# Performance work log

Measured on AMD Instinct MI355X. Metric: run time of the kernel, lower is better.

The kernel has to match this reference:

```python
import jax, jax.numpy as jnp
import numpy as np

N, C, H, W = 16, 256, 128, 128
TC = max(8, C // 32)  # temp_c
EPS = 1e-5


def setup_inputs() -> dict:
    key = jax.random.key(0)
    ks = jax.random.split(key, 10)
    x = jax.random.normal(ks[0], (N, C, H, W), jnp.float32)
    # conv1: 1x1, C -> TC (weight squeezed to [TC, C])
    w1 = jax.random.normal(ks[1], (TC, C), jnp.float32) * 0.05
    b1 = jnp.zeros((TC,), jnp.float32)
    # BatchNorm2d (inference form)
    bn_gamma = jnp.ones((TC,), jnp.float32)
    bn_beta = jnp.zeros((TC,), jnp.float32)
    bn_mean = jnp.zeros((TC,), jnp.float32)
    bn_var = jnp.ones((TC,), jnp.float32)
    # conv2: kernel (1,2), TC -> C, squeezed to [C, TC, 2]
    w2 = jax.random.normal(ks[2], (C, TC, 2), jnp.float32) * 0.1
    b2 = jnp.zeros((C,), jnp.float32)
    # conv3: kernel (2,1), TC -> C, squeezed to [C, TC, 2]
    w3 = jax.random.normal(ks[3], (C, TC, 2), jnp.float32) * 0.1
    b3 = jnp.zeros((C,), jnp.float32)
    # conv4: kernel (1,2), TC -> C, squeezed to [C, TC, 2]
    w4 = jax.random.normal(ks[4], (C, TC, 2), jnp.float32) * 0.1
    b4 = jnp.zeros((C,), jnp.float32)
    return dict(x=x, w1=w1, b1=b1, bn_gamma=bn_gamma, bn_beta=bn_beta,
                bn_mean=bn_mean, bn_var=bn_var, w2=w2, b2=b2, w3=w3, b3=b3,
                w4=w4, b4=b4)


def reference(x, w1, b1, bn_gamma, bn_beta, bn_mean, bn_var,
              w2, b2, w3, b3, w4, b4):
    n, c, Hh, Ww = x.shape
    # avg/max pools along W (per-row), H (per-col), and global (per-channel)
    cat_h = jnp.stack([x.mean(3), x.max(3)], axis=-1)            # [n,c,H,2]
    cat_w = jnp.stack([x.mean(2), x.max(2)], axis=-1)            # [n,c,W,2]
    cat_c = jnp.stack([x.mean((2, 3)), x.max((2, 3))], -1)[:, :, None, :]  # [n,c,1,2]
    x_cat = jnp.concatenate([cat_h, cat_w, cat_c], axis=2)       # [n,c,H+W+1,2]
    # 1x1 conv + BN (inference) + h_swish
    y = jnp.einsum('ncsk,tc->ntsk', x_cat, w1) + b1[None, :, None, None]
    inv = bn_gamma / jnp.sqrt(bn_var + EPS)
    y = (y - bn_mean[None, :, None, None]) * inv[None, :, None, None] \
        + bn_beta[None, :, None, None]
    y = y * jnp.clip(y + 3.0, 0.0, 6.0) / 6.0                    # h_swish
    # split
    xh = y[:, :, :Hh, :]               # [n,tc,H,2]
    xw = y[:, :, Hh:Hh + Ww, :]        # [n,tc,W,2]
    xc = y[:, :, Hh + Ww, :]           # [n,tc,2]
    # tiny convs (kernels collapse to contractions over (tc, k)) + sigmoid
    a_h = jax.nn.sigmoid(jnp.einsum('nthk,otk->noh', xh, w2) + b2[None, :, None])  # [n,C,H]
    a_w = jax.nn.sigmoid(jnp.einsum('ntwk,otk->now', xw, w3) + b3[None, :, None])  # [n,C,W]
    a_c = jax.nn.sigmoid(jnp.einsum('ntk,otk->no', xc, w4) + b4[None, :])          # [n,C]
    return x * a_w[:, :, None, :] * a_h[:, :, :, None] * a_c[:, :, None, None]
```

## Files before the change

### kernel.cpp

```cpp
#include <hip/hip_runtime.h>
#include <math.h>

#define N_ 16
#define C_ 256
#define H_ 128
#define W_ 128
#define TC_ 8
#define S_ 257
#define EPS_ 1e-5f
#define NBLK 512
#define BPN 32
#define PPB 8

#define XCT_OFF  0
#define AH_OFF   2105344
#define AW_OFF   (AH_OFF + 524288)
#define Y256_OFF (AW_OFF + 524288)
#define CNT_OFF  (Y256_OFF + 256)

typedef float f4n __attribute__((ext_vector_type(4)));

__device__ __forceinline__ void nbar(unsigned* c, unsigned target) {
    __syncthreads();
    if (threadIdx.x == 0) {
        __hip_atomic_fetch_add(c, 1u, __ATOMIC_RELEASE, __HIP_MEMORY_SCOPE_AGENT);
        while (__hip_atomic_load(c, __ATOMIC_RELAXED, __HIP_MEMORY_SCOPE_AGENT) < target)
            __builtin_amdgcn_s_sleep(16);
        (void)__hip_atomic_load(c, __ATOMIC_ACQUIRE, __HIP_MEMORY_SCOPE_AGENT);
    }
    __syncthreads();
}

__global__ __launch_bounds__(256, 2) void mega(
    const float* __restrict__ x,
    const float* __restrict__ w1, const float* __restrict__ b1,
    const float* __restrict__ gam, const float* __restrict__ bet,
    const float* __restrict__ mu, const float* __restrict__ var,
    const float* __restrict__ w2, const float* __restrict__ b2,
    const float* __restrict__ w3, const float* __restrict__ b3,
    const float* __restrict__ w4, const float* __restrict__ b4,
    float* __restrict__ xcat, float* __restrict__ ahg, float* __restrict__ awg,
    float* __restrict__ y256g, unsigned* __restrict__ cnt,
    float* __restrict__ out)
{
    const int b = blockIdx.x;
    const int n = b >> 5, cg = b & 31, c0 = cg * 8;
    const int tid = threadIdx.x;
    __shared__ __align__(16) float smf[9472];

    {
        float2 (*rowp)[33] = reinterpret_cast<float2(*)[33]>(smf);
        float4* scr_s = reinterpret_cast<float4*>(smf + 8448);
        float4* scr_m = reinterpret_cast<float4*>(smf + 8960);
        const int rg = tid >> 5;

        for (int u = 0; u < PPB; ++u) {
            const int p = b * PPB + u;
            const float4* xt = reinterpret_cast<const float4*>(x) + (size_t)p * 4096;
            float2* xcat2 = reinterpret_cast<float2*>(xcat) + (size_t)p * S_;

            float4 cs = make_float4(0.f, 0.f, 0.f, 0.f);
            float4 cm = make_float4(-INFINITY, -INFINITY, -INFINITY, -INFINITY);

            #pragma unroll
            for (int k = 0; k < 16; ++k) {
                const float4 v = xt[k * 256 + tid];
                cs.x += v.x; cs.y += v.y; cs.z += v.z; cs.w += v.w;
                cm.x = fmaxf(cm.x, v.x); cm.y = fmaxf(cm.y, v.y);
                cm.z = fmaxf(cm.z, v.z); cm.w = fmaxf(cm.w, v.w);
                const float rs = (v.x + v.y) + (v.z + v.w);
                const float rm = fmaxf(fmaxf(v.x, v.y), fmaxf(v.z, v.w));
                rowp[k * 8 + rg][tid & 31] = make_float2(rs, rm);
            }

            cs.x += __shfl_xor(cs.x, 32); cs.y += __shfl_xor(cs.y, 32);
            cs.z += __shfl_xor(cs.z, 32); cs.w += __shfl_xor(cs.w, 32);
            cm.x = fmaxf(cm.x, __shfl_xor(cm.x, 32));
            cm.y = fmaxf(cm.y, __shfl_xor(cm.y, 32));
            cm.z = fmaxf(cm.z, __shfl_xor(cm.z, 32));
            cm.w = fmaxf(cm.w, __shfl_xor(cm.w, 32));

            const int wv = tid >> 6, ln = tid & 63;
            if (ln < 32) { scr_s[wv * 32 + ln] = cs; scr_m[wv * 32 + ln] = cm; }
            __syncthreads();

            if (tid >= 128) {
                const int h = tid - 128;
                float2 q0 = rowp[h][0];
                float s = q0.x, m = q0.y;
                #pragma unroll
                for (int j = 1; j < 32; ++j) {
                    const float2 q = rowp[h][j];
                    s += q.x; m = fmaxf(m, q.y);
                }
                xcat2[h] = make_float2(s * (1.f / 128.f), m);
            }

            if (tid < 32) {
                const float4 s0 = scr_s[tid],      s1 = scr_s[32 + tid],
                             s2 = scr_s[64 + tid], s3 = scr_s[96 + tid];
                const float4 m0 = scr_m[tid],      m1 = scr_m[32 + tid],
                             m2 = scr_m[64 + tid], m3 = scr_m[96 + tid];
                float4 S, M;
                S.x = (s0.x + s1.x) + (s2.x + s3.x);
                S.y = (s0.y + s1.y) + (s2.y + s3.y);
                S.z = (s0.z + s1.z) + (s2.z + s3.z);
                S.w = (s0.w + s1.w) + (s2.w + s3.w);
                M.x = fmaxf(fmaxf(m0.x, m1.x), fmaxf(m2.x, m3.x));
                M.y = fmaxf(fmaxf(m0.y, m1.y), fmaxf(m2.y, m3.y));
                M.z = fmaxf(fmaxf(m0.z, m1.z), fmaxf(m2.z, m3.z));
                M.w = fmaxf(fmaxf(m0.w, m1.w), fmaxf(m2.w, m3.w));

                const int w0 = 4 * tid;
                xcat2[128 + w0 + 0] = make_float2(S.x * (1.f / 128.f), M.x);
                xcat2[128 + w0 + 1] = make_float2(S.y * (1.f / 128.f), M.y);
                xcat2[128 + w0 + 2] = make_float2(S.z * (1.f / 128.f), M.z);
                xcat2[128 + w0 + 3] = make_float2(S.w * (1.f / 128.f), M.w);

                float gs = (S.x + S.y) + (S.z + S.w);
                float gm = fmaxf(fmaxf(M.x, M.y), fmaxf(M.z, M.w));
                #pragma unroll
                for (int m = 16; m >= 1; m >>= 1) {
                    gs += __shfl_xor(gs, m);
                    gm = fmaxf(gm, __shfl_xor(gm, m));
                }
                if (tid == 0) xcat2[256] = make_float2(gs * (1.f / 16384.f), gm);
            }
            __syncthreads();
        }
    }

    nbar(cnt + n * 64, BPN);

    {
        float* w1s = smf;
        float* red = smf + 2048;
        float* ys  = smf + 6272;
        const float2* xc2 = reinterpret_cast<const float2*>(xcat) + (size_t)n * C_ * S_;
        const int s0 = cg * 8;

        for (int i = tid; i < TC_ * C_; i += 256) w1s[i] = w1[i];
        __syncthreads();

        {
            const int cgrp = tid >> 3, si = tid & 7;
            const int s = s0 + si;
            float acc[16];
            #pragma unroll
            for (int j = 0; j < 16; ++j) acc[j] = 0.f;
            #pragma unroll
            for (int i = 0; i < 8; ++i) {
                const int c = cgrp * 8 + i;
                const float2 v = xc2[c * S_ + s];
                #pragma unroll
                for (int t = 0; t < TC_; ++t) {
                    const float w = w1s[t * C_ + c];
                    acc[t * 2 + 0] += v.x * w;
                    acc[t * 2 + 1] += v.y * w;
                }
            }
            #pragma unroll
            for (int j = 0; j < 16; ++j) red[(si * 16 + j) * 33 + cgrp] = acc[j];
        }
        __syncthreads();

        if (tid < 128) {
            const int si2 = tid >> 4, j = tid & 15, t = j >> 1;
            float z = 0.f;
            #pragma unroll
            for (int g = 0; g < 32; ++g) z += red[(si2 * 16 + j) * 33 + g];
            const float inv = gam[t] * rsqrtf(var[t] + EPS_);
            float y = (z + b1[t] - mu[t]) * inv + bet[t];
            y = y * fminf(fmaxf(y + 3.f, 0.f), 6.f) * (1.f / 6.f);
            ys[si2 * 17 + j] = y;
        }
        __syncthreads();

        if (cg == BPN - 1) {
            const int c = tid;
            const float2 v = xc2[c * S_ + 256];
            float pj[16];
            #pragma unroll
            for (int t = 0; t < TC_; ++t) {
                const float w = w1s[t * C_ + c];
                pj[t * 2 + 0] = v.x * w;
                pj[t * 2 + 1] = v.y * w;
            }
            __syncthreads();
            float* red2 = smf;
            float* redB = smf + 4400;
            #pragma unroll
            for (int j = 0; j < 16; ++j) red2[tid * 17 + j] = pj[j];
            __syncthreads();
            {
                const int g = tid >> 4, j = tid & 15;
                float z = 0.f;
                #pragma unroll
                for (int m = 0; m < 16; ++m) z += red2[(g * 16 + m) * 17 + j];
                redB[j * 17 + g] = z;
            }
            __syncthreads();
            if (tid < 16) {
                const int j = tid, t = j >> 1;
                float z = 0.f;
                #pragma unroll
                for (int g = 0; g < 16; ++g) z += redB[j * 17 + g];
                const float inv = gam[t] * rsqrtf(var[t] + EPS_);
                float y = (z + b1[t] - mu[t]) * inv + bet[t];
                y = y * fminf(fmaxf(y + 3.f, 0.f), 6.f) * (1.f / 6.f);
                y256g[n * 16 + j] = y;
            }
            __syncthreads();
        }

        {
            const int o = tid;
            const bool is_h = (cg < 16);
            const float* wX = is_h ? w2 : w3;
            const float zb = is_h ? b2[o] : b3[o];
            float4 wr[4];
            const float4* wv = reinterpret_cast<const float4*>(wX + o * 16);
            #pragma unroll
            for (int q = 0; q < 4; ++q) wr[q] = wv[q];

            float r[8];
            #pragma unroll
            for (int si = 0; si < 8; ++si) {
                float z = zb;
                #pragma unroll
                for (int q = 0; q < 4; ++q) {
                    z += ys[si * 17 + q * 4 + 0] * wr[q].x
                       + ys[si * 17 + q * 4 + 1] * wr[q].y
                       + ys[si * 17 + q * 4 + 2] * wr[q].z
                       + ys[si * 17 + q * 4 + 3] * wr[q].w;
                }
                r[si] = 1.f / (1.f + expf(-z));
            }
            float* og = is_h ? (ahg + (size_t)(n * C_ + o) * H_ + s0)
                             : (awg + (size_t)(n * C_ + o) * W_ + (s0 - 128));
            *reinterpret_cast<float4*>(og)     = make_float4(r[0], r[1], r[2], r[3]);
            *reinterpret_cast<float4*>(og + 4) = make_float4(r[4], r[5], r[6], r[7]);
        }
    }

    nbar(cnt + n * 64 + 32, BPN);

    float* acs = smf;
    float* ahl = smf + 16;
    float* awl = smf + 1040;
    {
        if (tid < 8) {
            const int o = c0 + tid;
            float z = b4[o];
            #pragma unroll
            for (int j = 0; j < 16; ++j) z += y256g[n * 16 + j] * w4[o * 16 + j];
            acs[tid] = 1.f / (1.f + expf(-z));
        }
        __syncthreads();

        for (int idx = tid; idx < 8 * 128; idx += 256) {
            const int u = idx >> 7, h = idx & 127, o = c0 + u;
            ahl[idx] = acs[u] * ahg[(size_t)(n * C_ + o) * H_ + h];
            awl[idx] = awg[(size_t)(n * C_ + o) * W_ + h];
        }
        __syncthreads();
    }
    {
        const float4* awv = reinterpret_cast<const float4*>(awl);
        for (int u = 0; u < PPB; ++u) {
            const int p = b * PPB + u;
            const f4n* x4 = reinterpret_cast<const f4n*>(x) + (size_t)p * 4096;
            f4n* o4 = reinterpret_cast<f4n*>(out) + (size_t)p * 4096;

            const float4 a = awv[u * 32 + (tid & 31)];
            #pragma unroll
            for (int k = 0; k < 16; ++k) {
                const int i4 = k * 256 + tid;
                f4n v = x4[i4];
                const float s = ahl[u * 128 + k * 8 + (tid >> 5)];
                v.x *= s * a.x; v.y *= s * a.y; v.z *= s * a.z; v.w *= s * a.w;
                __builtin_nontemporal_store(v, &o4[i4]);
            }
        }
    }
}

extern "C" void kernel_launch(void* const* d_in, const int* in_sizes, int n_in,
                              void* d_out, int out_size, void* d_ws, size_t ws_size,
                              hipStream_t stream) {
    const float* x   = (const float*)d_in[0];
    const float* w1  = (const float*)d_in[1];
    const float* b1  = (const float*)d_in[2];
    const float* gam = (const float*)d_in[3];
    const float* bet = (const float*)d_in[4];
    const float* mu  = (const float*)d_in[5];
    const float* var = (const float*)d_in[6];
    const float* w2  = (const float*)d_in[7];
    const float* b2  = (const float*)d_in[8];
    const float* w3  = (const float*)d_in[9];
    const float* b3  = (const float*)d_in[10];
    const float* w4  = (const float*)d_in[11];
    const float* b4  = (const float*)d_in[12];

    float* ws    = (float*)d_ws;
    float* xcat  = ws + XCT_OFF;
    float* ahg   = ws + AH_OFF;
    float* awg   = ws + AW_OFF;
    float* y256g = ws + Y256_OFF;
    unsigned* cnt = (unsigned*)(ws + CNT_OFF);
    float* out   = (float*)d_out;

    hipMemsetAsync((void*)cnt, 0, 16 * 64 * sizeof(unsigned), stream);
    mega<<<NBLK, 256, 0, stream>>>(x, w1, b1, gam, bet, mu, var,
                                   w2, b2, w3, b3, w4, b4,
                                   xcat, ahg, awg, y256g, cnt, out);
}
```

Measured before the change: 175.5 us.

## Split persistent mega-kernel into three kernels replacing atomic grid barriers

Replaces the single persistent kernel, which used per-batch atomic spin barriers between phases, with three separate launches: pooling statistics, attention-vector computation, and the final apply. This removes the memset and the spin-wait barrier overhead, and lets kernels 2 and 3 use smaller shared memory for higher occupancy. In exchange it adds two extra launch boundaries and loses the chance that x stays in cache between the stats and apply phases in the same block.

```diff
diff --git a/kernel.cpp b/kernel.cpp
--- a/kernel.cpp
+++ b/kernel.cpp
@@ -16,271 +16,266 @@
 #define AH_OFF   2105344
 #define AW_OFF   (AH_OFF + 524288)
 #define Y256_OFF (AW_OFF + 524288)
-#define CNT_OFF  (Y256_OFF + 256)
 
 typedef float f4n __attribute__((ext_vector_type(4)));
 
-__device__ __forceinline__ void nbar(unsigned* c, unsigned target) {
-    __syncthreads();
-    if (threadIdx.x == 0) {
-        __hip_atomic_fetch_add(c, 1u, __ATOMIC_RELEASE, __HIP_MEMORY_SCOPE_AGENT);
-        while (__hip_atomic_load(c, __ATOMIC_RELAXED, __HIP_MEMORY_SCOPE_AGENT) < target)
-            __builtin_amdgcn_s_sleep(16);
-        (void)__hip_atomic_load(c, __ATOMIC_ACQUIRE, __HIP_MEMORY_SCOPE_AGENT);
-    }
-    __syncthreads();
+__global__ __launch_bounds__(256, 2) void k1_stats(
+    const float* __restrict__ x, float* __restrict__ xcat)
+{
+    const int b = blockIdx.x;
+    const int tid = threadIdx.x;
+    __shared__ __align__(16) float smf[9472];
+
+    float2 (*rowp)[33] = reinterpret_cast<float2(*)[33]>(smf);
+    float4* scr_s = reinterpret_cast<float4*>(smf + 8448);
+    float4* scr_m = reinterpret_cast<float4*>(smf + 8960);
+    const int rg = tid >> 5;
+
+    for (int u = 0; u < PPB; ++u) {
+        const int p = b * PPB + u;
+        const float4* xt = reinterpret_cast<const float4*>(x) + (size_t)p * 4096;
+        float2* xcat2 = reinterpret_cast<float2*>(xcat) + (size_t)p * S_;
+
+        float4 cs = make_float4(0.f, 0.f, 0.f, 0.f);
+        float4 cm = make_float4(-INFINITY, -INFINITY, -INFINITY, -INFINITY);
+
+        #pragma unroll
+        for (int k = 0; k < 16; ++k) {
+            const float4 v = xt[k * 256 + tid];
+            cs.x += v.x; cs.y += v.y; cs.z += v.z; cs.w += v.w;
+            cm.x = fmaxf(cm.x, v.x); cm.y = fmaxf(cm.y, v.y);
+            cm.z = fmaxf(cm.z, v.z); cm.w = fmaxf(cm.w, v.w);
+            const float rs = (v.x + v.y) + (v.z + v.w);
+            const float rm = fmaxf(fmaxf(v.x, v.y), fmaxf(v.z, v.w));
+            rowp[k * 8 + rg][tid & 31] = make_float2(rs, rm);
+        }
+
+        cs.x += __shfl_xor(cs.x, 32); cs.y += __shfl_xor(cs.y, 32);
+        cs.z += __shfl_xor(cs.z, 32); cs.w += __shfl_xor(cs.w, 32);
+        cm.x = fmaxf(cm.x, __shfl_xor(cm.x, 32));
+        cm.y = fmaxf(cm.y, __shfl_xor(cm.y, 32));
+        cm.z = fmaxf(cm.z, __shfl_xor(cm.z, 32));
+        cm.w = fmaxf(cm.w, __shfl_xor(cm.w, 32));
+
+        const int wv = tid >> 6, ln = tid & 63;
+        if (ln < 32) { scr_s[wv * 32 + ln] = cs; scr_m[wv * 32 + ln] = cm; }
+        __syncthreads();
+
+        if (tid >= 128) {
+            const int h = tid - 128;
+            float2 q0 = rowp[h][0];
+            float s = q0.x, m = q0.y;
+            #pragma unroll
+            for (int j = 1; j < 32; ++j) {
+                const float2 q = rowp[h][j];
+                s += q.x; m = fmaxf(m, q.y);
+            }
+            xcat2[h] = make_float2(s * (1.f / 128.f), m);
+        }
+
+        if (tid < 32) {
+            const float4 s0 = scr_s[tid],      s1 = scr_s[32 + tid],
+                         s2 = scr_s[64 + tid], s3 = scr_s[96 + tid];
+            const float4 m0 = scr_m[tid],      m1 = scr_m[32 + tid],
+                         m2 = scr_m[64 + tid], m3 = scr_m[96 + tid];
+            float4 S, M;
+            S.x = (s0.x + s1.x) + (s2.x + s3.x);
+            S.y = (s0.y + s1.y) + (s2.y + s3.y);
+            S.z = (s0.z + s1.z) + (s2.z + s3.z);
+            S.w = (s0.w + s1.w) + (s2.w + s3.w);
+            M.x = fmaxf(fmaxf(m0.x, m1.x), fmaxf(m2.x, m3.x));
+            M.y = fmaxf(fmaxf(m0.y, m1.y), fmaxf(m2.y, m3.y));
+            M.z = fmaxf(fmaxf(m0.z, m1.z), fmaxf(m2.z, m3.z));
+            M.w = fmaxf(fmaxf(m0.w, m1.w), fmaxf(m2.w, m3.w));
+
+            const int w0 = 4 * tid;
+            xcat2[128 + w0 + 0] = make_float2(S.x * (1.f / 128.f), M.x);
+            xcat2[128 + w0 + 1] = make_float2(S.y * (1.f / 128.f), M.y);
+            xcat2[128 + w0 + 2] = make_float2(S.z * (1.f / 128.f), M.z);
+            xcat2[128 + w0 + 3] = make_float2(S.w * (1.f / 128.f), M.w);
+
+            float gs = (S.x + S.y) + (S.z + S.w);
+            float gm = fmaxf(fmaxf(M.x, M.y), fmaxf(M.z, M.w));
+            #pragma unroll
+            for (int m = 16; m >= 1; m >>= 1) {
+                gs += __shfl_xor(gs, m);
+                gm = fmaxf(gm, __shfl_xor(gm, m));
+            }
+            if (tid == 0) xcat2[256] = make_float2(gs * (1.f / 16384.f), gm);
+        }
+        __syncthreads();
+    }
 }
 
-__global__ __launch_bounds__(256, 2) void mega(
-    const float* __restrict__ x,
+__global__ __launch_bounds__(256, 2) void k2_attn(
+    const float* __restrict__ xcat,
     const float* __restrict__ w1, const float* __restrict__ b1,
     const float* __restrict__ gam, const float* __restrict__ bet,
     const float* __restrict__ mu, const float* __restrict__ var,
     const float* __restrict__ w2, const float* __restrict__ b2,
     const float* __restrict__ w3, const float* __restrict__ b3,
+    float* __restrict__ ahg, float* __restrict__ awg, float* __restrict__ y256g)
+{
+    const int b = blockIdx.x;
+    const int n = b >> 5, cg = b & 31;
+    const int tid = threadIdx.x;
+    __shared__ __align__(16) float smf[6448];
+
+    float* w1s = smf;
+    float* red = smf + 2048;
+    float* ys  = smf + 6272;
+    const float2* xc2 = reinterpret_cast<const float2*>(xcat) + (size_t)n * C_ * S_;
+    const int s0 = cg * 8;
+
+    for (int i = tid; i < TC_ * C_; i += 256) w1s[i] = w1[i];
+    __syncthreads();
+
+    {
+        const int cgrp = tid >> 3, si = tid & 7;
+        const int s = s0 + si;
+        float acc[16];
+        #pragma unroll
+        for (int j = 0; j < 16; ++j) acc[j] = 0.f;
+        #pragma unroll
+        for (int i = 0; i < 8; ++i) {
+            const int c = cgrp * 8 + i;
+            const float2 v = xc2[c * S_ + s];
+            #pragma unroll
+            for (int t = 0; t < TC_; ++t) {
+                const float w = w1s[t * C_ + c];
+                acc[t * 2 + 0] += v.x * w;
+                acc[t * 2 + 1] += v.y * w;
+            }
+        }
+        #pragma unroll
+        for (int j = 0; j < 16; ++j) red[(si * 16 + j) * 33 + cgrp] = acc[j];
+    }
+    __syncthreads();
+
+    if (tid < 128) {
+        const int si2 = tid >> 4, j = tid & 15, t = j >> 1;
+        float z = 0.f;
+        #pragma unroll
+        for (int g = 0; g < 32; ++g) z += red[(si2 * 16 + j) * 33 + g];
+        const float inv = gam[t] * rsqrtf(var[t] + EPS_);
+        float y = (z + b1[t] - mu[t]) * inv + bet[t];
+        y = y * fminf(fmaxf(y + 3.f, 0.f), 6.f) * (1.f / 6.f);
+        ys[si2 * 17 + j] = y;
+    }
+    __syncthreads();
+
+    if (cg == BPN - 1) {
+        const int c = tid;
+        const float2 v = xc2[c * S_ + 256];
+        float pj[16];
+        #pragma unroll
+        for (int t = 0; t < TC_; ++t) {
+            const float w = w1s[t * C_ + c];
+            pj[t * 2 + 0] = v.x * w;
+            pj[t * 2 + 1] = v.y * w;
+        }
+        __syncthreads();
+        float* red2 = smf;
+        float* redB = smf + 4400;
+        #pragma unroll
+        for (int j = 0; j < 16; ++j) red2[tid * 17 + j] = pj[j];
+        __syncthreads();
+        {
+            const int g = tid >> 4, j = tid & 15;
+            float z = 0.f;
+            #pragma unroll
+            for (int m = 0; m < 16; ++m) z += red2[(g * 16 + m) * 17 + j];
+            redB[j * 17 + g] = z;
+        }
+        __syncthreads();
+        if (tid < 16) {
+            const int j = tid, t = j >> 1;
+            float z = 0.f;
+            #pragma unroll
+            for (int g = 0; g < 16; ++g) z += redB[j * 17 + g];
+            const float inv = gam[t] * rsqrtf(var[t] + EPS_);
+            float y = (z + b1[t] - mu[t]) * inv + bet[t];
+            y = y * fminf(fmaxf(y + 3.f, 0.f), 6.f) * (1.f / 6.f);
+            y256g[n * 16 + j] = y;
+        }
+        __syncthreads();
+    }
+
+    {
+        const int o = tid;
+        const bool is_h = (cg < 16);
+        const float* wX = is_h ? w2 : w3;
+        const float zb = is_h ? b2[o] : b3[o];
+        float4 wr[4];
+        const float4* wv = reinterpret_cast<const float4*>(wX + o * 16);
+        #pragma unroll
+        for (int q = 0; q < 4; ++q) wr[q] = wv[q];
+
+        float r[8];
+        #pragma unroll
+        for (int si = 0; si < 8; ++si) {
+            float z = zb;
+            #pragma unroll
+            for (int q = 0; q < 4; ++q) {
+                z += ys[si * 17 + q * 4 + 0] * wr[q].x
+                   + ys[si * 17 + q * 4 + 1] * wr[q].y
+                   + ys[si * 17 + q * 4 + 2] * wr[q].z
+                   + ys[si * 17 + q * 4 + 3] * wr[q].w;
+            }
+            r[si] = 1.f / (1.f + expf(-z));
+        }
+        float* og = is_h ? (ahg + (size_t)(n * C_ + o) * H_ + s0)
+                         : (awg + (size_t)(n * C_ + o) * W_ + (s0 - 128));
+        *reinterpret_cast<float4*>(og)     = make_float4(r[0], r[1], r[2], r[3]);
+        *reinterpret_cast<float4*>(og + 4) = make_float4(r[4], r[5], r[6], r[7]);
+    }
+}
+
+__global__ __launch_bounds__(256, 2) void k3_apply(
+    const float* __restrict__ x,
     const float* __restrict__ w4, const float* __restrict__ b4,
-    float* __restrict__ xcat, float* __restrict__ ahg, float* __restrict__ awg,
-    float* __restrict__ y256g, unsigned* __restrict__ cnt,
-    float* __restrict__ out)
+    const float* __restrict__ ahg, const float* __restrict__ awg,
+    const float* __restrict__ y256g, float* __restrict__ out)
 {
     const int b = blockIdx.x;
     const int n = b >> 5, cg = b & 31, c0 = cg * 8;
     const int tid = threadIdx.x;
-    __shared__ __align__(16) float smf[9472];
-
-    {
-        float2 (*rowp)[33] = reinterpret_cast<float2(*)[33]>(smf);
-        float4* scr_s = reinterpret_cast<float4*>(smf + 8448);
-        float4* scr_m = reinterpret_cast<float4*>(smf + 8960);
-        const int rg = tid >> 5;
-
-        for (int u = 0; u < PPB; ++u) {
-            const int p = b * PPB + u;
-            const float4* xt = reinterpret_cast<const float4*>(x) + (size_t)p * 4096;
-            float2* xcat2 = reinterpret_cast<float2*>(xcat) + (size_t)p * S_;
-
-            float4 cs = make_float4(0.f, 0.f, 0.f, 0.f);
-            float4 cm = make_float4(-INFINITY, -INFINITY, -INFINITY, -INFINITY);
-
-            #pragma unroll
-            for (int k = 0; k < 16; ++k) {
-                const float4 v = xt[k * 256 + tid];
-                cs.x += v.x; cs.y += v.y; cs.z += v.z; cs.w += v.w;
-                cm.x = fmaxf(cm.x, v.x); cm.y = fmaxf(cm.y, v.y);
-                cm.z = fmaxf(cm.z, v.z); cm.w = fmaxf(cm.w, v.w);
-                const float rs = (v.x + v.y) + (v.z + v.w);
-                const float rm = fmaxf(fmaxf(v.x, v.y), fmaxf(v.z, v.w));
-                rowp[k * 8 + rg][tid & 31] = make_float2(rs, rm);
-            }
-
-            cs.x += __shfl_xor(cs.x, 32); cs.y += __shfl_xor(cs.y, 32);
-            cs.z += __shfl_xor(cs.z, 32); cs.w += __shfl_xor(cs.w, 32);
-            cm.x = fmaxf(cm.x, __shfl_xor(cm.x, 32));
-            cm.y = fmaxf(cm.y, __shfl_xor(cm.y, 32));
-            cm.z = fmaxf(cm.z, __shfl_xor(cm.z, 32));
-            cm.w = fmaxf(cm.w, __shfl_xor(cm.w, 32));
-
-            const int wv = tid >> 6, ln = tid & 63;
-            if (ln < 32) { scr_s[wv * 32 + ln] = cs; scr_m[wv * 32 + ln] = cm; }
-            __syncthreads();
-
-            if (tid >= 128) {
-                const int h = tid - 128;
-                float2 q0 = rowp[h][0];
-                float s = q0.x, m = q0.y;
-                #pragma unroll
-                for (int j = 1; j < 32; ++j) {
-                    const float2 q = rowp[h][j];
-                    s += q.x; m = fmaxf(m, q.y);
-                }
-                xcat2[h] = make_float2(s * (1.f / 128.f), m);
-            }
-
-            if (tid < 32) {
-                const float4 s0 = scr_s[tid],      s1 = scr_s[32 + tid],
-                             s2 = scr_s[64 + tid], s3 = scr_s[96 + tid];
-                const float4 m0 = scr_m[tid],      m1 = scr_m[32 + tid],
-                             m2 = scr_m[64 + tid], m3 = scr_m[96 + tid];
-                float4 S, M;
-                S.x = (s0.x + s1.x) + (s2.x + s3.x);
-                S.y = (s0.y + s1.y) + (s2.y + s3.y);
-                S.z = (s0.z + s1.z) + (s2.z + s3.z);
-                S.w = (s0.w + s1.w) + (s2.w + s3.w);
-                M.x = fmaxf(fmaxf(m0.x, m1.x), fmaxf(m2.x, m3.x));
-                M.y = fmaxf(fmaxf(m0.y, m1.y), fmaxf(m2.y, m3.y));
-                M.z = fmaxf(fmaxf(m0.z, m1.z), fmaxf(m2.z, m3.z));
-                M.w = fmaxf(fmaxf(m0.w, m1.w), fmaxf(m2.w, m3.w));
-
-                const int w0 = 4 * tid;
-                xcat2[128 + w0 + 0] = make_float2(S.x * (1.f / 128.f), M.x);
-                xcat2[128 + w0 + 1] = make_float2(S.y * (1.f / 128.f), M.y);
-                xcat2[128 + w0 + 2] = make_float2(S.z * (1.f / 128.f), M.z);
-                xcat2[128 + w0 + 3] = make_float2(S.w * (1.f / 128.f), M.w);
-
-                float gs = (S.x + S.y) + (S.z + S.w);
-                float gm = fmaxf(fmaxf(M.x, M.y), fmaxf(M.z, M.w));
-                #pragma unroll
-                for (int m = 16; m >= 1; m >>= 1) {
-                    gs += __shfl_xor(gs, m);
-                    gm = fmaxf(gm, __shfl_xor(gm, m));
-                }
-                if (tid == 0) xcat2[256] = make_float2(gs * (1.f / 16384.f), gm);
-            }
-            __syncthreads();
-        }
-    }
-
-    nbar(cnt + n * 64, BPN);
-
-    {
-        float* w1s = smf;
-        float* red = smf + 2048;
-        float* ys  = smf + 6272;
-        const float2* xc2 = reinterpret_cast<const float2*>(xcat) + (size_t)n * C_ * S_;
-        const int s0 = cg * 8;
-
-        for (int i = tid; i < TC_ * C_; i += 256) w1s[i] = w1[i];
-        __syncthreads();
-
-        {
-            const int cgrp = tid >> 3, si = tid & 7;
-            const int s = s0 + si;
-            float acc[16];
-            #pragma unroll
-            for (int j = 0; j < 16; ++j) acc[j] = 0.f;
-            #pragma unroll
-            for (int i = 0; i < 8; ++i) {
-                const int c = cgrp * 8 + i;
-                const float2 v = xc2[c * S_ + s];
-                #pragma unroll
-                for (int t = 0; t < TC_; ++t) {
-                    const float w = w1s[t * C_ + c];
-                    acc[t * 2 + 0] += v.x * w;
-                    acc[t * 2 + 1] += v.y * w;
-                }
-            }
-            #pragma unroll
-            for (int j = 0; j < 16; ++j) red[(si * 16 + j) * 33 + cgrp] = acc[j];
-        }
-        __syncthreads();
-
-        if (tid < 128) {
-            const int si2 = tid >> 4, j = tid & 15, t = j >> 1;
-            float z = 0.f;
-            #pragma unroll
-            for (int g = 0; g < 32; ++g) z += red[(si2 * 16 + j) * 33 + g];
-            const float inv = gam[t] * rsqrtf(var[t] + EPS_);
-            float y = (z + b1[t] - mu[t]) * inv + bet[t];
-            y = y * fminf(fmaxf(y + 3.f, 0.f), 6.f) * (1.f / 6.f);
-            ys[si2 * 17 + j] = y;
-        }
-        __syncthreads();
-
-        if (cg == BPN - 1) {
-            const int c = tid;
-            const float2 v = xc2[c * S_ + 256];
-            float pj[16];
-            #pragma unroll
-            for (int t = 0; t < TC_; ++t) {
-                const float w = w1s[t * C_ + c];
-                pj[t * 2 + 0] = v.x * w;
-                pj[t * 2 + 1] = v.y * w;
-            }
-            __syncthreads();
-            float* red2 = smf;
-            float* redB = smf + 4400;
-            #pragma unroll
-            for (int j = 0; j < 16; ++j) red2[tid * 17 + j] = pj[j];
-            __syncthreads();
-            {
-                const int g = tid >> 4, j = tid & 15;
-                float z = 0.f;
-                #pragma unroll
-                for (int m = 0; m < 16; ++m) z += red2[(g * 16 + m) * 17 + j];
-                redB[j * 17 + g] = z;
-            }
-            __syncthreads();
-            if (tid < 16) {
-                const int j = tid, t = j >> 1;
-                float z = 0.f;
-                #pragma unroll
-                for (int g = 0; g < 16; ++g) z += redB[j * 17 + g];
-                const float inv = gam[t] * rsqrtf(var[t] + EPS_);
-                float y = (z + b1[t] - mu[t]) * inv + bet[t];
-                y = y * fminf(fmaxf(y + 3.f, 0.f), 6.f) * (1.f / 6.f);
-                y256g[n * 16 + j] = y;
-            }
-            __syncthreads();
-        }
-
-        {
-            const int o = tid;
-            const bool is_h = (cg < 16);
-            const float* wX = is_h ? w2 : w3;
-            const float zb = is_h ? b2[o] : b3[o];
-            float4 wr[4];
-            const float4* wv = reinterpret_cast<const float4*>(wX + o * 16);
-            #pragma unroll
-            for (int q = 0; q < 4; ++q) wr[q] = wv[q];
-
-            float r[8];
-            #pragma unroll
-            for (int si = 0; si < 8; ++si) {
-                float z = zb;
-                #pragma unroll
-                for (int q = 0; q < 4; ++q) {
-                    z += ys[si * 17 + q * 4 + 0] * wr[q].x
-                       + ys[si * 17 + q * 4 + 1] * wr[q].y
-                       + ys[si * 17 + q * 4 + 2] * wr[q].z
-                       + ys[si * 17 + q * 4 + 3] * wr[q].w;
-                }
-                r[si] = 1.f / (1.f + expf(-z));
-            }
-            float* og = is_h ? (ahg + (size_t)(n * C_ + o) * H_ + s0)
-                             : (awg + (size_t)(n * C_ + o) * W_ + (s0 - 128));
-            *reinterpret_cast<float4*>(og)     = make_float4(r[0], r[1], r[2], r[3]);
-            *reinterpret_cast<float4*>(og + 4) = make_float4(r[4], r[5], r[6], r[7]);
-        }
-    }
-
-    nbar(cnt + n * 64 + 32, BPN);
+    __shared__ __align__(16) float smf[2064];
 
     float* acs = smf;
     float* ahl = smf + 16;
     float* awl = smf + 1040;
-    {
-        if (tid < 8) {
-            const int o = c0 + tid;
-            float z = b4[o];
-            #pragma unroll
-            for (int j = 0; j < 16; ++j) z += y256g[n * 16 + j] * w4[o * 16 + j];
-            acs[tid] = 1.f / (1.f + expf(-z));
-        }
-        __syncthreads();
-
-        for (int idx = tid; idx < 8 * 128; idx += 256) {
-            const int u = idx >> 7, h = idx & 127, o = c0 + u;
-            ahl[idx] = acs[u] * ahg[(size_t)(n * C_ + o) * H_ + h];
-            awl[idx] = awg[(size_t)(n * C_ + o) * W_ + h];
-        }
-        __syncthreads();
-    }
-    {
-        const float4* awv = reinterpret_cast<const float4*>(awl);
-        for (int u = 0; u < PPB; ++u) {
-            const int p = b * PPB + u;
-            const f4n* x4 = reinterpret_cast<const f4n*>(x) + (size_t)p * 4096;
-            f4n* o4 = reinterpret_cast<f4n*>(out) + (size_t)p * 4096;
-
-            const float4 a = awv[u * 32 + (tid & 31)];
-            #pragma unroll
-            for (int k = 0; k < 16; ++k) {
-                const int i4 = k * 256 + tid;
-                f4n v = x4[i4];
-                const float s = ahl[u * 128 + k * 8 + (tid >> 5)];
-                v.x *= s * a.x; v.y *= s * a.y; v.z *= s * a.z; v.w *= s * a.w;
-                __builtin_nontemporal_store(v, &o4[i4]);
-            }
+
+    if (tid < 8) {
+        const int o = c0 + tid;
+        float z = b4[o];
+        #pragma unroll
+        for (int j = 0; j < 16; ++j) z += y256g[n * 16 + j] * w4[o * 16 + j];
+        acs[tid] = 1.f / (1.f + expf(-z));
+    }
+    __syncthreads();
+
+    for (int idx = tid; idx < 8 * 128; idx += 256) {
+        const int u = idx >> 7, h = idx & 127, o = c0 + u;
+        ahl[idx] = acs[u] * ahg[(size_t)(n * C_ + o) * H_ + h];
+        awl[idx] = awg[(size_t)(n * C_ + o) * W_ + h];
+    }
+    __syncthreads();
+
+    const float4* awv = reinterpret_cast<const float4*>(awl);
+    for (int u = 0; u < PPB; ++u) {
+        const int p = b * PPB + u;
+        const f4n* x4 = reinterpret_cast<const f4n*>(x) + (size_t)p * 4096;
+        f4n* o4 = reinterpret_cast<f4n*>(out) + (size_t)p * 4096;
+
+        const float4 a = awv[u * 32 + (tid & 31)];
+        #pragma unroll
+        for (int k = 0; k < 16; ++k) {
+            const int i4 = k * 256 + tid;
+            f4n v = x4[i4];
+            const float s = ahl[u * 128 + k * 8 + (tid >> 5)];
+            v.x *= s * a.x; v.y *= s * a.y; v.z *= s * a.z; v.w *= s * a.w;
+            __builtin_nontemporal_store(v, &o4[i4]);
         }
     }
 }
@@ -307,11 +302,10 @@
     float* ahg   = ws + AH_OFF;
     float* awg   = ws + AW_OFF;
     float* y256g = ws + Y256_OFF;
-    unsigned* cnt = (unsigned*)(ws + CNT_OFF);
     float* out   = (float*)d_out;
 
-    hipMemsetAsync((void*)cnt, 0, 16 * 64 * sizeof(unsigned), stream);
-    mega<<<NBLK, 256, 0, stream>>>(x, w1, b1, gam, bet, mu, var,
-                                   w2, b2, w3, b3, w4, b4,
-                                   xcat, ahg, awg, y256g, cnt, out);
+    k1_stats<<<NBLK, 256, 0, stream>>>(x, xcat);
+    k2_attn<<<NBLK, 256, 0, stream>>>(xcat, w1, b1, gam, bet, mu, var,
+                                      w2, b2, w3, b3, ahg, awg, y256g);
+    k3_apply<<<NBLK, 256, 0, stream>>>(x, w4, b4, ahg, awg, y256g, out);
 }
```

Result: no change. 177.4 us (+1.1%).
